# Performance work log

Measured on AMD Instinct MI355X. Metric: run time of the kernel, lower is better.

Reference implementation:

```python
import jax, jax.numpy as jnp
import numpy as np

B, N, D = 256, 196, 1024   # batch, regions, vis_embed_dim
HID, ATT, SIN, WID, ISD = 1024, 256, 1024, 1024, 256
S = 10                      # sentence steps


def _lin(key, out_dim, in_dim):
    kw, kb = jax.random.split(key)
    w = jax.random.normal(kw, (out_dim, in_dim), jnp.float32) * 0.02
    b = jax.random.normal(kb, (out_dim,), jnp.float32) * 0.02
    return w, b


def setup_inputs() -> dict:
    key = jax.random.key(0)
    ks = jax.random.split(key, 16)
    inp = {}
    inp['vis_enc'] = jax.random.normal(ks[0], (B, N, D), jnp.float32)
    inp['sentences'] = jax.random.randint(ks[1], (B, S, 50), 0, 10000, jnp.int64)
    inp['enc_att_w'], inp['enc_att_b'] = _lin(ks[2], ATT, D)
    inp['dec_att_w'], inp['dec_att_b'] = _lin(ks[3], ATT, HID)
    inp['full_att_w'], inp['full_att_b'] = _lin(ks[4], 1, ATT)
    inp['ctx_w'], inp['ctx_b'] = _lin(ks[5], SIN, D)
    inp['W_ih'], inp['b_ih'] = _lin(ks[6], 4 * HID, SIN)
    inp['W_hh'], inp['b_hh'] = _lin(ks[7], 4 * HID, HID)
    inp['topic_hid_w'], inp['topic_hid_b'] = _lin(ks[8], WID, HID)
    inp['topic_ctx_w'], inp['topic_ctx_b'] = _lin(ks[9], WID, SIN)
    inp['stop_prev_w'], inp['stop_prev_b'] = _lin(ks[10], ISD, HID)
    inp['stop_cur_w'], inp['stop_cur_b'] = _lin(ks[11], ISD, HID)
    inp['final_stop_w'], inp['final_stop_b'] = _lin(ks[12], 2, ISD)
    return inp


def reference(vis_enc, sentences,
              enc_att_w, enc_att_b, dec_att_w, dec_att_b, full_att_w, full_att_b,
              ctx_w, ctx_b, W_ih, b_ih, W_hh, b_hh,
              topic_hid_w, topic_hid_b, topic_ctx_w, topic_ctx_b,
              stop_prev_w, stop_prev_b, stop_cur_w, stop_cur_b,
              final_stop_w, final_stop_b):
    batch, hid = vis_enc.shape[0], W_hh.shape[1]
    sent_num = sentences.shape[1]
    # encoder projection is h-independent -> hoist out of the recurrence
    vis_enc_att = jnp.einsum('bnd,ad->bna', vis_enc, enc_att_w) + enc_att_b  # [B,N,ATT]

    def step(carry, _):
        h, c = carry
        # CoAtt additive attention
        dec = h @ dec_att_w.T + dec_att_b                       # [B,ATT]
        join = jnp.tanh(vis_enc_att + dec[:, None, :])          # [B,N,ATT]
        logits = jnp.einsum('bna,a->bn', join, full_att_w[0]) + full_att_b[0]
        scores = jax.nn.softmax(logits, axis=1)                 # [B,N]
        att_out = jnp.einsum('bn,bnd->bd', scores, vis_enc)     # [B,D]
        ctx = att_out @ ctx_w.T + ctx_b                         # [B,SIN]
        h_prev = h
        # LSTMCell
        gates = ctx @ W_ih.T + b_ih + h @ W_hh.T + b_hh         # [B,4H]
        i, f, g, o = jnp.split(gates, 4, axis=1)
        c_new = jax.nn.sigmoid(f) * c + jax.nn.sigmoid(i) * jnp.tanh(g)
        h_new = jax.nn.sigmoid(o) * jnp.tanh(c_new)
        # topic + stop heads
        topic = jnp.tanh(h_new @ topic_hid_w.T + topic_hid_b
                         + ctx @ topic_ctx_w.T + topic_ctx_b)   # [B,WID]
        p = jnp.tanh(h_prev @ stop_prev_w.T + stop_prev_b
                     + h_new @ stop_cur_w.T + stop_cur_b)
        p = p @ final_stop_w.T + final_stop_b                   # [B,2]
        return (h_new, c_new), (topic, p)

    h0 = jnp.zeros((batch, hid), vis_enc.dtype)
    c0 = jnp.zeros((batch, hid), vis_enc.dtype)
    _, (topics, ps) = jax.lax.scan(step, (h0, c0), None, length=sent_num)
    topics = jnp.transpose(topics, (1, 0, 2))  # [B,S,WID]
    ps = jnp.transpose(ps, (1, 0, 2))          # [B,S,2]
    return topics, ps
```

## Files before the change

### kernel.cpp

```cpp
#include <hip/hip_runtime.h>
#include <hip/hip_bf16.h>
#include <math.h>

static constexpr int BB = 256;
static constexpr int NR = 196;
static constexpr int DV = 1024;
static constexpr int HH = 1024;
static constexpr int AT = 256;
static constexpr int SI = 1024;
static constexpr int WI = 1024;
static constexpr int IS = 256;
static constexpr int ST = 10;

__device__ __forceinline__ float sigmoidf_(float x) { return 1.0f / (1.0f + expf(-x)); }

__device__ __forceinline__ ushort f2bf(float x) {
    uint u = __float_as_uint(x);
    return (ushort)((u + 0x7FFFu + ((u >> 16) & 1u)) >> 16);
}
__device__ __forceinline__ float bf2f(ushort b) { return __uint_as_float(((uint)b) << 16); }

using bf16x8 = __attribute__((ext_vector_type(8))) short;
using f32x4  = __attribute__((ext_vector_type(4))) float;
#define MFMA_B16(a, b, c) __builtin_amdgcn_mfma_f32_16x16x32_bf16((a), (b), (c), 0, 0, 0)

__device__ __forceinline__ void split8(const float4& u, const float4& v, uint4& hq, uint4& lq) {
    ushort h0 = f2bf(u.x), h1 = f2bf(u.y), h2 = f2bf(u.z), h3 = f2bf(u.w);
    ushort h4 = f2bf(v.x), h5 = f2bf(v.y), h6 = f2bf(v.z), h7 = f2bf(v.w);
    hq.x = h0 | ((uint)h1 << 16); hq.y = h2 | ((uint)h3 << 16);
    hq.z = h4 | ((uint)h5 << 16); hq.w = h6 | ((uint)h7 << 16);
    ushort l0 = f2bf(u.x - bf2f(h0)), l1 = f2bf(u.y - bf2f(h1));
    ushort l2 = f2bf(u.z - bf2f(h2)), l3 = f2bf(u.w - bf2f(h3));
    ushort l4 = f2bf(v.x - bf2f(h4)), l5 = f2bf(v.y - bf2f(h5));
    ushort l6 = f2bf(v.z - bf2f(h6)), l7 = f2bf(v.w - bf2f(h7));
    lq.x = l0 | ((uint)l1 << 16); lq.y = l2 | ((uint)l3 << 16);
    lq.z = l4 | ((uint)l5 << 16); lq.w = l6 | ((uint)l7 << 16);
}

struct CvtTab { const float* s[5]; ushort* h[5]; ushort* l[5]; };

__global__ __launch_bounds__(256) void convert_split(CvtTab tab) {
    const int cum[6] = {0, 256, 4352, 5376, 5632, 5888};
    const int bid = blockIdx.x;
    int seg = 0;
#pragma unroll
    for (int i = 1; i < 5; ++i) if (bid >= cum[i]) seg = i;
    const float* s = tab.s[seg];
    ushort* h = tab.h[seg];
    ushort* l = tab.l[seg];
    const int r = bid - cum[seg];
    int rd = r;
    if (seg == 1) rd = (r & 1023) * 4 + (r >> 10);
    const int src = r * 1024 + threadIdx.x * 4;
    const size_t dst = (size_t)rd * 1024 + threadIdx.x * 4;
    float4 v = *(const float4*)(s + src);
    ushort h0 = f2bf(v.x), h1 = f2bf(v.y), h2 = f2bf(v.z), h3 = f2bf(v.w);
    uint2 hq, lq;
    hq.x = h0 | ((uint)h1 << 16); hq.y = h2 | ((uint)h3 << 16);
    ushort l0 = f2bf(v.x - bf2f(h0)), l1 = f2bf(v.y - bf2f(h1));
    ushort l2 = f2bf(v.z - bf2f(h2)), l3 = f2bf(v.w - bf2f(h3));
    lq.x = l0 | ((uint)l1 << 16); lq.y = l2 | ((uint)l3 << 16);
    *(uint2*)(h + dst) = hq;
    *(uint2*)(l + dst) = lq;
}

__global__ __launch_bounds__(256) void convert_vis(
    const float* __restrict__ src, ushort* __restrict__ dst)
{
    const size_t i = ((size_t)blockIdx.x * 256 + threadIdx.x) * 8;
    const float4 v0 = *(const float4*)(src + i);
    const float4 v1 = *(const float4*)(src + i + 4);
    uint4 o;
    o.x = f2bf(v0.x) | ((uint)f2bf(v0.y) << 16);
    o.y = f2bf(v0.z) | ((uint)f2bf(v0.w) << 16);
    o.z = f2bf(v1.x) | ((uint)f2bf(v1.y) << 16);
    o.w = f2bf(v1.z) | ((uint)f2bf(v1.w) << 16);
    *(uint4*)(dst + i) = o;
}

__global__ __launch_bounds__(256) void transpose_split(
    const float* __restrict__ src, ushort* __restrict__ dh, ushort* __restrict__ dl)
{
    __shared__ float T[32][33];
    const int tx = threadIdx.x & 31, ty = threadIdx.x >> 5;
    const int k0 = blockIdx.x * 32, n0 = blockIdx.y * 32;
#pragma unroll
    for (int j = 0; j < 4; ++j)
        T[ty + 8 * j][tx] = src[(size_t)(k0 + ty + 8 * j) * 1024 + n0 + tx];
    __syncthreads();
#pragma unroll
    for (int j = 0; j < 4; ++j) {
        const float v = T[tx][ty + 8 * j];
        const ushort h = f2bf(v);
        const size_t o = (size_t)(n0 + ty + 8 * j) * 1024 + k0 + tx;
        dh[o] = h;
        dl[o] = f2bf(v - bf2f(h));
    }
}

__global__ __launch_bounds__(256) void foldbias(
    const float* __restrict__ W, const float* __restrict__ v,
    const float* __restrict__ b, float* __restrict__ out)
{
    const int n = blockIdx.x * 4 + (threadIdx.x >> 6);
    const int lane = threadIdx.x & 63;
    const float* wr = W + (size_t)n * 1024;
    float p = 0.f;
#pragma unroll
    for (int i = 0; i < 4; ++i) {
        const float4 wv = *(const float4*)&wr[i * 256 + lane * 4];
        const float4 vv = *(const float4*)&v[i * 256 + lane * 4];
        p = fmaf(wv.x, vv.x, p); p = fmaf(wv.y, vv.y, p);
        p = fmaf(wv.z, vv.z, p); p = fmaf(wv.w, vv.w, p);
    }
    for (int off = 32; off; off >>= 1) p += __shfl_down(p, off);
    if (lane == 0) out[n] = p + b[n];
}

template <int ILV>
__global__ __launch_bounds__(256) void mgemm_ws(
    const float* __restrict__ A, const ushort* __restrict__ Wh, const ushort* __restrict__ Wl,
    ushort* __restrict__ Ch, ushort* __restrict__ Cl, int N, int K)
{
    __shared__ __align__(16) ushort SM[4 * 64 * 40];
    ushort* Ah = SM; ushort* Al = SM + 2560; ushort* Bh = SM + 5120; ushort* Bl = SM + 7680;

    const int t = threadIdx.x;
    const int m0 = blockIdx.y * 64, n0 = blockIdx.x * 64;
    const int w = t >> 6, lane = t & 63;
    const int l15 = lane & 15, q = lane >> 4;
    const int sr = t >> 2, sq = (t & 3) * 8;
    const int nch = K >> 5;

    f32x4 acc[4] = {};
    float4 pa0, pa1; uint4 pbh, pbl;
    auto pref = [&](int c) {
        const int k0 = c << 5;
        const float* ap = &A[(size_t)(m0 + sr) * K + k0 + sq];
        pa0 = *(const float4*)ap;
        pa1 = *(const float4*)(ap + 4);
        pbh = *(const uint4*)&Wh[(size_t)(n0 + sr) * K + k0 + sq];
        pbl = *(const uint4*)&Wl[(size_t)(n0 + sr) * K + k0 + sq];
    };
    pref(0);

    for (int c = 0; c < nch; ++c) {
        __syncthreads();
        uint4 hq, lq; split8(pa0, pa1, hq, lq);
        *(uint4*)&Ah[sr * 40 + sq] = hq;
        *(uint4*)&Al[sr * 40 + sq] = lq;
        *(uint4*)&Bh[sr * 40 + sq] = pbh;
        *(uint4*)&Bl[sr * 40 + sq] = pbl;
        __syncthreads();
        if (c + 1 < nch) pref(c + 1);
        const bf16x8 bh = *(const bf16x8*)&Bh[(w * 16 + l15) * 40 + q * 8];
        const bf16x8 bl = *(const bf16x8*)&Bl[(w * 16 + l15) * 40 + q * 8];
#pragma unroll
        for (int mi = 0; mi < 4; ++mi) {
            const bf16x8 ah = *(const bf16x8*)&Ah[(mi * 16 + l15) * 40 + q * 8];
            const bf16x8 al = *(const bf16x8*)&Al[(mi * 16 + l15) * 40 + q * 8];
            acc[mi] = MFMA_B16(ah, bh, acc[mi]);
            acc[mi] = MFMA_B16(ah, bl, acc[mi]);
            acc[mi] = MFMA_B16(al, bh, acc[mi]);
        }
    }

    const int col = n0 + w * 16 + l15;
#pragma unroll
    for (int mi = 0; mi < 4; ++mi) {
#pragma unroll
        for (int j = 0; j < 4; ++j) {
            const int row = m0 + mi * 16 + q * 4 + j;
            const int ro = ILV ? ((row & 1023) * 4 + (row >> 10)) : row;
            const float v = acc[mi][j];
            const ushort h = f2bf(v);
            Ch[(size_t)ro * N + col] = h;
            Cl[(size_t)ro * N + col] = f2bf(v - bf2f(h));
        }
    }
}

template <int EPI, int DUAL, int OMAP>
__global__ __launch_bounds__(256) void mgemm(
    const float* __restrict__ A1, const ushort* __restrict__ W1h, const ushort* __restrict__ W1l,
    const float* __restrict__ b1,
    const float* __restrict__ A2, const ushort* __restrict__ W2h, const ushort* __restrict__ W2l,
    const float* __restrict__ b2,
    float* __restrict__ C, int M, int N, int K, int ldc)
{
    __shared__ __align__(16) ushort SM[4 * 64 * 40];
    ushort* Ah = SM; ushort* Al = SM + 2560; ushort* Bh = SM + 5120; ushort* Bl = SM + 7680;

    const int t = threadIdx.x;
    const int m0 = blockIdx.y * 64, n0 = blockIdx.x * 64;
    const int w = t >> 6, lane = t & 63;
    const int l15 = lane & 15, q = lane >> 4;
    const int sr = t >> 2, sq = (t & 3) * 8;
    const int KC = K >> 5, nch = (DUAL ? 2 : 1) * KC;

    f32x4 acc[4] = {};
    float4 pa0, pa1; uint4 pbh, pbl;

    auto pref = [&](int c) {
        const int pass = DUAL ? (c >= KC ? 1 : 0) : 0;
        const int k0 = (c - pass * KC) << 5;
        const float* A = pass ? A2 : A1;
        const ushort* Wh = pass ? W2h : W1h;
        const ushort* Wl = pass ? W2l : W1l;
        const float* ap = &A[(size_t)(m0 + sr) * K + k0 + sq];
        pa0 = *(const float4*)ap;
        pa1 = *(const float4*)(ap + 4);
        pbh = *(const uint4*)&Wh[(size_t)(n0 + sr) * K + k0 + sq];
        pbl = *(const uint4*)&Wl[(size_t)(n0 + sr) * K + k0 + sq];
    };
    pref(0);

    for (int c = 0; c < nch; ++c) {
        __syncthreads();
        uint4 hq, lq; split8(pa0, pa1, hq, lq);
        *(uint4*)&Ah[sr * 40 + sq] = hq;
        *(uint4*)&Al[sr * 40 + sq] = lq;
        *(uint4*)&Bh[sr * 40 + sq] = pbh;
        *(uint4*)&Bl[sr * 40 + sq] = pbl;
        __syncthreads();
        if (c + 1 < nch) pref(c + 1);
        const bf16x8 bh = *(const bf16x8*)&Bh[(w * 16 + l15) * 40 + q * 8];
        const bf16x8 bl = *(const bf16x8*)&Bl[(w * 16 + l15) * 40 + q * 8];
#pragma unroll
        for (int mi = 0; mi < 4; ++mi) {
            const bf16x8 ah = *(const bf16x8*)&Ah[(mi * 16 + l15) * 40 + q * 8];
            const bf16x8 al = *(const bf16x8*)&Al[(mi * 16 + l15) * 40 + q * 8];
            acc[mi] = MFMA_B16(ah, bh, acc[mi]);
            acc[mi] = MFMA_B16(ah, bl, acc[mi]);
            acc[mi] = MFMA_B16(al, bh, acc[mi]);
        }
    }

    const int col = n0 + w * 16 + l15;
    float bias = b1[col];
    if (DUAL) bias += b2[col];
#pragma unroll
    for (int mi = 0; mi < 4; ++mi) {
#pragma unroll
        for (int j = 0; j < 4; ++j) {
            const int row = m0 + mi * 16 + q * 4 + j;
            float v = acc[mi][j] + bias;
            if (EPI == 1) v = tanhf(v);
            if (OMAP)
                C[((size_t)(row & 255) * ST + (row >> 8)) * ldc + col] = v;
            else
                C[(size_t)row * ldc + col] = v;
        }
    }
}

__global__ __launch_bounds__(512) void mgemm8_lstm(
    const ushort* __restrict__ A1h, const ushort* __restrict__ A1l,
    const ushort* __restrict__ W1h, const ushort* __restrict__ W1l,
    const float* __restrict__ b1,
    const ushort* __restrict__ A2h, const ushort* __restrict__ A2l,
    const ushort* __restrict__ W2h, const ushort* __restrict__ W2l,
    const float* __restrict__ b2,
    int K, float* __restrict__ cvec, float* __restrict__ hnew,
    ushort* __restrict__ hnh, ushort* __restrict__ hnl)
{
    __shared__ __align__(16) ushort SM[32256];

    const int t = threadIdx.x;
    const int m0 = blockIdx.y * 64, n0 = blockIdx.x * 32;
    const int w = t >> 6, lane = t & 63;
    const int g = w >> 2, wg = w & 3;
    const int l15 = lane & 15, q = lane >> 4;
    const int tl = t & 255;
    const int sr = tl >> 2, sq4 = (tl & 3) * 16;
    const int br = tl >> 3, bq = (tl & 7) * 8;
    const int mh = wg >> 1;
    const int colL = (wg & 1) * 16 + l15;

    ushort* Ah = SM + g * 13824;
    ushort* Al = Ah + 4608;
    ushort* Bh = Al + 4608;
    ushort* Bl = Bh + 2304;

    const int nchg = K >> 6;
    const ushort* Ahg = g ? A2h : A1h;
    const ushort* Alg = g ? A2l : A1l;
    const ushort* Wh  = g ? W2h : W1h;
    const ushort* Wl  = g ? W2l : W1l;

    f32x4 acc[2] = {};
    uint4 pah0, pah1, pal0, pal1, pbh, pbl;
    auto pref = [&](int c) {
        const int k0 = c << 6;
        const size_t ab = (size_t)(m0 + sr) * K + k0 + sq4;
        pah0 = *(const uint4*)&Ahg[ab];
        pah1 = *(const uint4*)&Ahg[ab + 8];
        pal0 = *(const uint4*)&Alg[ab];
        pal1 = *(const uint4*)&Alg[ab + 8];
        pbh = *(const uint4*)&Wh[(size_t)(n0 + br) * K + k0 + bq];
        pbl = *(const uint4*)&Wl[(size_t)(n0 + br) * K + k0 + bq];
    };
    pref(0);

    for (int c = 0; c < nchg; ++c) {
        __syncthreads();
        *(uint4*)&Ah[sr * 72 + sq4]     = pah0;
        *(uint4*)&Ah[sr * 72 + sq4 + 8] = pah1;
        *(uint4*)&Al[sr * 72 + sq4]     = pal0;
        *(uint4*)&Al[sr * 72 + sq4 + 8] = pal1;
        *(uint4*)&Bh[br * 72 + bq] = pbh;
        *(uint4*)&Bl[br * 72 + bq] = pbl;
        __syncthreads();
        if (c + 1 < nchg) pref(c + 1);
#pragma unroll
        for (int ks = 0; ks < 2; ++ks) {
            const bf16x8 bh = *(const bf16x8*)&Bh[colL * 72 + ks * 32 + q * 8];
            const bf16x8 bl = *(const bf16x8*)&Bl[colL * 72 + ks * 32 + q * 8];
#pragma unroll
            for (int i = 0; i < 2; ++i) {
                const int mi = mh * 2 + i;
                const bf16x8 ah = *(const bf16x8*)&Ah[(mi * 16 + l15) * 72 + ks * 32 + q * 8];
                const bf16x8 al = *(const bf16x8*)&Al[(mi * 16 + l15) * 72 + ks * 32 + q * 8];
                acc[i] = MFMA_B16(ah, bh, acc[i]);
                acc[i] = MFMA_B16(ah, bl, acc[i]);
                acc[i] = MFMA_B16(al, bh, acc[i]);
            }
        }
    }

    float* comb = (float*)(SM + 27648);
    __syncthreads();
    if (g == 1) {
#pragma unroll
        for (int i = 0; i < 2; ++i)
#pragma unroll
            for (int j = 0; j < 4; ++j) comb[tl * 9 + i * 4 + j] = acc[i][j];
    }
    __syncthreads();
    if (g == 0) {
#pragma unroll
        for (int i = 0; i < 2; ++i)
#pragma unroll
            for (int j = 0; j < 4; ++j) acc[i][j] += comb[tl * 9 + i * 4 + j];
    }

    float* G = (float*)(SM + 13824);
    if (g == 0) {
        const int colG = n0 + colL;
        const int gate = colG & 3, unit = colG >> 2;
        const float bias = b1[gate * 1024 + unit] + b2[gate * 1024 + unit];
#pragma unroll
        for (int i = 0; i < 2; ++i) {
            const int mi = mh * 2 + i;
#pragma unroll
            for (int j = 0; j < 4; ++j)
                G[(mi * 16 + q * 4 + j) * 40 + colL] = acc[i][j] + bias;
        }
    }
    __syncthreads();
    {
        const int row = t >> 3, ul = t & 7;
        const float4 g4 = *(const float4*)&G[row * 40 + ul * 4];
        const size_t ci = (size_t)(m0 + row) * HH + (n0 >> 2) + ul;
        const float cn = sigmoidf_(g4.y) * cvec[ci] + sigmoidf_(g4.x) * tanhf(g4.z);
        cvec[ci] = cn;
        const float hv = sigmoidf_(g4.w) * tanhf(cn);
        hnew[ci] = hv;
        const ushort hhi = f2bf(hv);
        hnh[ci] = hhi;
        hnl[ci] = f2bf(hv - bf2f(hhi));
    }
}

__global__ __launch_bounds__(256) void mgemm_preb(
    const ushort* __restrict__ vh, const ushort* __restrict__ Wh, const ushort* __restrict__ Wl,
    const float* __restrict__ bias, ushort* __restrict__ C)
{
    __shared__ __align__(16) ushort Avh[64 * 40];
    __shared__ __align__(16) ushort Bh[256 * 40];
    __shared__ __align__(16) ushort Bl[256 * 40];

    const int t = threadIdx.x;
    const int m0 = blockIdx.x * 64;
    const int w = t >> 6, lane = t & 63;
    const int l15 = lane & 15, q = lane >> 4;
    const int ar = t >> 2, ac = (t & 3) * 8;
    const int K = DV;

    f32x4 acc[4][4] = {};

    for (int c = 0; c < 32; ++c) {
        const int k0 = c << 5;
        __syncthreads();
        *(uint4*)&Avh[ar * 40 + ac] = *(const uint4*)&vh[(size_t)(m0 + ar) * K + k0 + ac];
#pragma unroll
        for (int j = 0; j < 4; ++j) {
            const int r = j * 64 + (t >> 2);
            *(uint4*)&Bh[r * 40 + ac] = *(const uint4*)&Wh[(size_t)r * K + k0 + ac];
            *(uint4*)&Bl[r * 40 + ac] = *(const uint4*)&Wl[(size_t)r * K + k0 + ac];
        }
        __syncthreads();

        bf16x8 ah[4];
#pragma unroll
        for (int mi = 0; mi < 4; ++mi)
            ah[mi] = *(const bf16x8*)&Avh[(mi * 16 + l15) * 40 + q * 8];
#pragma unroll
        for (int ni = 0; ni < 4; ++ni) {
            const bf16x8 bh = *(const bf16x8*)&Bh[(w * 64 + ni * 16 + l15) * 40 + q * 8];
            const bf16x8 bl = *(const bf16x8*)&Bl[(w * 64 + ni * 16 + l15) * 40 + q * 8];
#pragma unroll
            for (int mi = 0; mi < 4; ++mi) {
                acc[mi][ni] = MFMA_B16(ah[mi], bh, acc[mi][ni]);
                acc[mi][ni] = MFMA_B16(ah[mi], bl, acc[mi][ni]);
            }
        }
    }

#pragma unroll
    for (int ni = 0; ni < 4; ++ni) {
        const int col = w * 64 + ni * 16 + l15;
        const float bb = bias[col];
#pragma unroll
        for (int mi = 0; mi < 4; ++mi)
#pragma unroll
            for (int j = 0; j < 4; ++j) {
                const int row = m0 + mi * 16 + q * 4 + j;
                C[(size_t)row * AT + col] = f2bf(acc[mi][ni][j] + bb);
            }
    }
}

__global__ __launch_bounds__(256) void mgemm_pre(
    const float* __restrict__ A, const ushort* __restrict__ Wh, const ushort* __restrict__ Wl,
    const float* __restrict__ bias, ushort* __restrict__ C)
{
    __shared__ __align__(16) ushort Ah[64 * 40], Al[64 * 40];
    __shared__ __align__(16) ushort Bh[256 * 40], Bl[256 * 40];

    const int t = threadIdx.x;
    const int m0 = blockIdx.x * 64;
    const int w = t >> 6, lane = t & 63;
    const int l15 = lane & 15, q = lane >> 4;
    const int sr = t >> 2, sq = (t & 3) * 8;
    const int K = DV;

    f32x4 acc[4][4] = {};
    float4 pa0, pa1;
    auto prefA = [&](int k0) {
        const float* ap = &A[(size_t)(m0 + sr) * K + k0 + sq];
        pa0 = *(const float4*)ap;
        pa1 = *(const float4*)(ap + 4);
    };
    prefA(0);

    for (int c = 0; c < 32; ++c) {
        const int k0 = c << 5;
        __syncthreads();
        uint4 hq, lq; split8(pa0, pa1, hq, lq);
        *(uint4*)&Ah[sr * 40 + sq] = hq;
        *(uint4*)&Al[sr * 40 + sq] = lq;
#pragma unroll
        for (int i = 0; i < 4; ++i) {
            const int r = sr + 64 * i;
            *(uint4*)&Bh[r * 40 + sq] = *(const uint4*)&Wh[(size_t)r * K + k0 + sq];
            *(uint4*)&Bl[r * 40 + sq] = *(const uint4*)&Wl[(size_t)r * K + k0 + sq];
        }
        __syncthreads();
        if (c + 1 < 32) prefA((c + 1) << 5);

        bf16x8 ah[4], al[4];
#pragma unroll
        for (int mi = 0; mi < 4; ++mi) {
            ah[mi] = *(const bf16x8*)&Ah[(mi * 16 + l15) * 40 + q * 8];
            al[mi] = *(const bf16x8*)&Al[(mi * 16 + l15) * 40 + q * 8];
        }
#pragma unroll
        for (int ni = 0; ni < 4; ++ni) {
            const bf16x8 bh = *(const bf16x8*)&Bh[(w * 64 + ni * 16 + l15) * 40 + q * 8];
            const bf16x8 bl = *(const bf16x8*)&Bl[(w * 64 + ni * 16 + l15) * 40 + q * 8];
#pragma unroll
            for (int mi = 0; mi < 4; ++mi) {
                acc[mi][ni] = MFMA_B16(ah[mi], bh, acc[mi][ni]);
                acc[mi][ni] = MFMA_B16(ah[mi], bl, acc[mi][ni]);
                acc[mi][ni] = MFMA_B16(al[mi], bh, acc[mi][ni]);
            }
        }
    }

#pragma unroll
    for (int ni = 0; ni < 4; ++ni) {
        const int col = w * 64 + ni * 16 + l15;
        const float bb = bias[col];
#pragma unroll
        for (int mi = 0; mi < 4; ++mi)
#pragma unroll
            for (int j = 0; j < 4; ++j) {
                const int row = m0 + mi * 16 + q * 4 + j;
                C[(size_t)row * AT + col] = f2bf(acc[mi][ni][j] + bb);
            }
    }
}

template <int VBF>
__global__ __launch_bounds__(1024) void att_step(
    const ushort* __restrict__ vis_att, const float* __restrict__ h,
    const float* __restrict__ dec_w, const float* __restrict__ dec_b,
    const float* __restrict__ fw, const float* __restrict__ fbp,
    const void* __restrict__ visp, float* __restrict__ att_out,
    ushort* __restrict__ att_h, ushort* __restrict__ att_l)
{
    const int b = blockIdx.x;
    const int t = threadIdx.x;
    const int lane = t & 63;
    const int w = t >> 6;

    __shared__ float hs[HH];
    __shared__ float decs[AT];
    __shared__ float fwv[AT];
    __shared__ float logit[NR + 4];
    __shared__ float sc[NR + 4];
    __shared__ float red[8];
    __shared__ float part[8][DV];

    hs[t] = h[(size_t)b * HH + t];
    if (t < AT) fwv[t] = fw[t];
    __syncthreads();
    const float fb = fbp[0];

#pragma unroll
    for (int j = 0; j < 16; ++j) {
        const int a = w * 16 + j;
        const float* wr = dec_w + (size_t)a * HH;
        float p = 0.f;
#pragma unroll
        for (int i = 0; i < 4; ++i) {
            const float4 wv = *(const float4*)&wr[i * 256 + lane * 4];
            const float4 hv = *(const float4*)&hs[i * 256 + lane * 4];
            p = fmaf(wv.x, hv.x, p); p = fmaf(wv.y, hv.y, p);
            p = fmaf(wv.z, hv.z, p); p = fmaf(wv.w, hv.w, p);
        }
        for (int off = 32; off; off >>= 1) p += __shfl_down(p, off);
        if (lane == 0) decs[a] = p + dec_b[a];
    }
    __syncthreads();

    for (int n = w; n < NR; n += 16) {
        const ushort4 v4 = *(const ushort4*)&vis_att[((size_t)b * NR + n) * AT + lane * 4];
        const int a = lane * 4;
        float s = tanhf(bf2f(v4.x) + decs[a]) * fwv[a];
        s = fmaf(tanhf(bf2f(v4.y) + decs[a + 1]), fwv[a + 1], s);
        s = fmaf(tanhf(bf2f(v4.z) + decs[a + 2]), fwv[a + 2], s);
        s = fmaf(tanhf(bf2f(v4.w) + decs[a + 3]), fwv[a + 3], s);
        for (int off = 32; off; off >>= 1) s += __shfl_down(s, off);
        if (lane == 0) logit[n] = s + fb;
    }
    __syncthreads();

    float m = -1e30f, e = 0.f;
    if (t < NR) m = logit[t];
    if (t < 256) {
        for (int off = 32; off; off >>= 1) m = fmaxf(m, __shfl_down(m, off));
        if (lane == 0) red[w] = m;
    }
    __syncthreads();
    m = fmaxf(fmaxf(red[0], red[1]), fmaxf(red[2], red[3]));
    if (t < NR) e = expf(logit[t] - m);
    if (t < 256) {
        float ss = e;
        for (int off = 32; off; off >>= 1) ss += __shfl_down(ss, off);
        if (lane == 0) red[4 + w] = ss;
    }
    __syncthreads();
    const float S = red[4] + red[5] + red[6] + red[7];
    if (t < NR) sc[t] = e / S;
    __syncthreads();

    const int slice = t >> 7;
    const int c8 = (t & 127) * 8;
    const int nbeg = (slice <= 4) ? 25 * slice : 100 + 24 * (slice - 4);
    const int nend = (slice < 4) ? nbeg + 25 : nbeg + 24;
    float a0 = 0.f, a1 = 0.f, a2 = 0.f, a3 = 0.f;
    float a4 = 0.f, a5 = 0.f, a6 = 0.f, a7 = 0.f;
    if (VBF) {
        const ushort* vb = (const ushort*)visp + (size_t)b * NR * DV + c8;
        for (int n = nbeg; n < nend; ++n) {
            const float s = sc[n];
            const uint4 v = *(const uint4*)&vb[(size_t)n * DV];
            a0 = fmaf(s, bf2f((ushort)(v.x & 0xFFFF)), a0);
            a1 = fmaf(s, bf2f((ushort)(v.x >> 16)), a1);
            a2 = fmaf(s, bf2f((ushort)(v.y & 0xFFFF)), a2);
            a3 = fmaf(s, bf2f((ushort)(v.y >> 16)), a3);
            a4 = fmaf(s, bf2f((ushort)(v.z & 0xFFFF)), a4);
            a5 = fmaf(s, bf2f((ushort)(v.z >> 16)), a5);
            a6 = fmaf(s, bf2f((ushort)(v.w & 0xFFFF)), a6);
            a7 = fmaf(s, bf2f((ushort)(v.w >> 16)), a7);
        }
    } else {
        const float* vb = (const float*)visp + (size_t)b * NR * DV + c8;
        for (int n = nbeg; n < nend; ++n) {
            const float s = sc[n];
            const float4 v0 = *(const float4*)&vb[(size_t)n * DV];
            const float4 v1 = *(const float4*)&vb[(size_t)n * DV + 4];
            a0 = fmaf(s, v0.x, a0); a1 = fmaf(s, v0.y, a1);
            a2 = fmaf(s, v0.z, a2); a3 = fmaf(s, v0.w, a3);
            a4 = fmaf(s, v1.x, a4); a5 = fmaf(s, v1.y, a5);
            a6 = fmaf(s, v1.z, a6); a7 = fmaf(s, v1.w, a7);
        }
    }
    float4 av0; av0.x = a0; av0.y = a1; av0.z = a2; av0.w = a3;
    float4 av1; av1.x = a4; av1.y = a5; av1.z = a6; av1.w = a7;
    *(float4*)&part[slice][c8]     = av0;
    *(float4*)&part[slice][c8 + 4] = av1;
    __syncthreads();
    const float v = ((part[0][t] + part[1][t]) + (part[2][t] + part[3][t]))
                  + ((part[4][t] + part[5][t]) + (part[6][t] + part[7][t]));
    att_out[(size_t)b * DV + t] = v;
    const ushort vh16 = f2bf(v);
    att_h[(size_t)b * DV + t] = vh16;
    att_l[(size_t)b * DV + t] = f2bf(v - bf2f(vh16));
}

__global__ __launch_bounds__(256) void stop_final_all(
    const float* __restrict__ pt, const float* __restrict__ fw,
    const float* __restrict__ fb, float* __restrict__ outp)
{
    const int row = blockIdx.x;
    const int s = row >> 8, b = row & 255;
    const int t = threadIdx.x;
    const int lane = t & 63;
    const int w = t >> 6;

    __shared__ float red[16];
    const float v = pt[(size_t)row * IS + t];
    float p0 = v * fw[t];
    float p1 = v * fw[IS + t];
    for (int off = 32; off; off >>= 1) {
        p0 += __shfl_down(p0, off);
        p1 += __shfl_down(p1, off);
    }
    if (lane == 0) { red[w] = p0; red[8 + w] = p1; }
    __syncthreads();
    if (t == 0) {
        outp[((size_t)b * ST + s) * 2 + 0] = red[0] + red[1] + red[2] + red[3] + fb[0];
        outp[((size_t)b * ST + s) * 2 + 1] = red[8] + red[9] + red[10] + red[11] + fb[1];
    }
}

extern "C" void kernel_launch(void* const* d_in, const int* in_sizes, int n_in,
                              void* d_out, int out_size, void* d_ws, size_t ws_size,
                              hipStream_t stream)
{
    const float* vis        = (const float*)d_in[0];
    const float* enc_att_w  = (const float*)d_in[2];
    const float* enc_att_b  = (const float*)d_in[3];
    const float* dec_att_w  = (const float*)d_in[4];
    const float* dec_att_b  = (const float*)d_in[5];
    const float* full_att_w = (const float*)d_in[6];
    const float* full_att_b = (const float*)d_in[7];
    const float* ctx_w      = (const float*)d_in[8];
    const float* ctx_b      = (const float*)d_in[9];
    const float* W_ih       = (const float*)d_in[10];
    const float* b_ih       = (const float*)d_in[11];
    const float* W_hh       = (const float*)d_in[12];
    const float* b_hh       = (const float*)d_in[13];
    const float* topic_hid_w = (const float*)d_in[14];
    const float* topic_hid_b = (const float*)d_in[15];
    const float* topic_ctx_w = (const float*)d_in[16];
    const float* topic_ctx_b = (const float*)d_in[17];
    const float* stop_prev_w = (const float*)d_in[18];
    const float* stop_prev_b = (const float*)d_in[19];
    const float* stop_cur_w  = (const float*)d_in[20];
    const float* stop_cur_b  = (const float*)d_in[21];
    const float* final_stop_w = (const float*)d_in[22];
    const float* final_stop_b = (const float*)d_in[23];

    float* out_topics = (float*)d_out;
    float* out_ps     = (float*)d_out + (size_t)BB * ST * WI;

    char* ws = (char*)d_ws;
    size_t off = 0;
    auto alloc = [&](size_t bytes) -> void* {
        void* p = (void*)(ws + off);
        off += (bytes + 255) & ~(size_t)255;
        return p;
    };
    ushort* vis_att = (ushort*)alloc((size_t)BB * NR * AT * 2);
    const size_t WTOT = (size_t)5888 * 1024;
    ushort* wh = (ushort*)alloc(WTOT * 2);
    ushort* wl = (ushort*)alloc(WTOT * 2);
    float* h_all   = (float*)alloc((size_t)(ST + 1) * BB * HH * 4);
    ushort* hh_h   = (ushort*)alloc((size_t)(ST + 1) * BB * HH * 2);
    ushort* hh_l   = (ushort*)alloc((size_t)(ST + 1) * BB * HH * 2);
    float* att_all = (float*)alloc((size_t)ST * BB * DV * 4);
    ushort* att_h  = (ushort*)alloc((size_t)BB * DV * 2);
    ushort* att_l  = (ushort*)alloc((size_t)BB * DV * 2);
    float* cbuf    = (float*)alloc((size_t)BB * HH * 4);
    float* pt_all  = (float*)alloc((size_t)ST * BB * IS * 4);
    ushort* ctT_h  = (ushort*)alloc((size_t)SI * DV * 2);
    ushort* ctT_l  = (ushort*)alloc((size_t)SI * DV * 2);
    ushort* cmb_h  = (ushort*)alloc((size_t)4 * HH * SI * 2);
    ushort* cmb_l  = (ushort*)alloc((size_t)4 * HH * SI * 2);
    ushort* tcc_h  = (ushort*)alloc((size_t)WI * SI * 2);
    ushort* tcc_l  = (ushort*)alloc((size_t)WI * SI * 2);
    float* bf_ih   = (float*)alloc((size_t)4 * HH * 4);
    float* bf_tc   = (float*)alloc((size_t)WI * 4);
    if (off > ws_size) return;
    ushort* vis_bf = nullptr;
    {
        const size_t need = (size_t)BB * NR * DV * 2;
        if (off + need <= ws_size) vis_bf = (ushort*)alloc(need);
    }

    const size_t O_ENC = 0;
    const size_t O_HH  = 262144;
    const size_t O_TH  = 4456448;
    const size_t O_SP  = 5505024;
    const size_t O_SC  = 5767168;

    CvtTab tab;
    const float* srcs[5] = {enc_att_w, W_hh, topic_hid_w, stop_prev_w, stop_cur_w};
    const size_t offs[5] = {O_ENC, O_HH, O_TH, O_SP, O_SC};
    for (int i = 0; i < 5; ++i) {
        tab.s[i] = srcs[i];
        tab.h[i] = wh + offs[i];
        tab.l[i] = wl + offs[i];
    }

    hipMemsetAsync(h_all, 0, (size_t)BB * HH * 4, stream);
    hipMemsetAsync(hh_h, 0, (size_t)BB * HH * 2, stream);
    hipMemsetAsync(hh_l, 0, (size_t)BB * HH * 2, stream);
    hipMemsetAsync(cbuf, 0, (size_t)BB * HH * 4, stream);

    convert_split<<<5888, 256, 0, stream>>>(tab);

    transpose_split<<<dim3(SI / 32, DV / 32), 256, 0, stream>>>(ctx_w, ctT_h, ctT_l);
    mgemm_ws<1><<<dim3(SI / 64, 4 * HH / 64), 256, 0, stream>>>(
        W_ih, ctT_h, ctT_l, cmb_h, cmb_l, SI, DV);
    mgemm_ws<0><<<dim3(SI / 64, WI / 64), 256, 0, stream>>>(
        topic_ctx_w, ctT_h, ctT_l, tcc_h, tcc_l, SI, DV);
    foldbias<<<(4 * HH) / 4, 256, 0, stream>>>(W_ih, ctx_b, b_ih, bf_ih);
    foldbias<<<WI / 4, 256, 0, stream>>>(topic_ctx_w, ctx_b, topic_ctx_b, bf_tc);

    if (vis_bf) {
        convert_vis<<<(BB * NR * DV) / (256 * 8), 256, 0, stream>>>(vis, vis_bf);
        mgemm_preb<<<(BB * NR) / 64, 256, 0, stream>>>(
            vis_bf, wh + O_ENC, wl + O_ENC, enc_att_b, vis_att);
    } else {
        mgemm_pre<<<(BB * NR) / 64, 256, 0, stream>>>(
            vis, wh + O_ENC, wl + O_ENC, enc_att_b, vis_att);
    }

    for (int s = 0; s < ST; ++s) {
        float* hc = h_all + (size_t)s * BB * HH;
        float* hn = h_all + (size_t)(s + 1) * BB * HH;
        ushort* hch = hh_h + (size_t)s * BB * HH;
        ushort* hcl = hh_l + (size_t)s * BB * HH;
        ushort* hnh = hh_h + (size_t)(s + 1) * BB * HH;
        ushort* hnl = hh_l + (size_t)(s + 1) * BB * HH;
        float* atts = att_all + (size_t)s * BB * DV;
        if (vis_bf)
            att_step<1><<<BB, 1024, 0, stream>>>(vis_att, hc, dec_att_w, dec_att_b,
                                                 full_att_w, full_att_b, vis_bf, atts,
                                                 att_h, att_l);
        else
            att_step<0><<<BB, 1024, 0, stream>>>(vis_att, hc, dec_att_w, dec_att_b,
                                                 full_att_w, full_att_b, vis, atts,
                                                 att_h, att_l);
        mgemm8_lstm<<<dim3(4 * HH / 32, BB / 64), 512, 0, stream>>>(
            att_h, att_l, cmb_h, cmb_l, bf_ih,
            hch, hcl, wh + O_HH, wl + O_HH, b_hh,
            SI, cbuf, hn, hnh, hnl);
    }

    mgemm<1, 1, 1><<<dim3(WI / 64, (ST * BB) / 64), 256, 0, stream>>>(
        h_all + (size_t)BB * HH, wh + O_TH, wl + O_TH, topic_hid_b,
        att_all, tcc_h, tcc_l, bf_tc,
        out_topics, ST * BB, WI, HH, WI);
    mgemm<1, 1, 0><<<dim3(IS / 64, (ST * BB) / 64), 256, 0, stream>>>(
        h_all, wh + O_SP, wl + O_SP, stop_prev_b,
        h_all + (size_t)BB * HH, wh + O_SC, wl + O_SC, stop_cur_b,
        pt_all, ST * BB, IS, HH, IS);
    stop_final_all<<<ST * BB, 256, 0, stream>>>(pt_all, final_stop_w, final_stop_b, out_ps);
}
```

Baseline: 1.099 ms.

## Enlarge encoder-projection GEMM tile to 128 rows and prefetch next K chunk

The bf16 encoder-attention projection kernel now uses 512 threads and a 128-row M tile, so each block shares the loaded weight tile (hi and lo parts) across twice as many rows. It also loads the next K chunk into registers before the current chunk's MFMAs, so global loads overlap with compute. This cuts redundant weight traffic from global memory, at the cost of more registers and half as many blocks. It only affects the one-time precompute ahead of the recurrence.

```diff
diff --git a/kernel.cpp b/kernel.cpp
--- a/kernel.cpp
+++ b/kernel.cpp
@@ -372,43 +372,54 @@
     }
 }
 
-__global__ __launch_bounds__(256) void mgemm_preb(
+__global__ __launch_bounds__(512) void mgemm_preb(
     const ushort* __restrict__ vh, const ushort* __restrict__ Wh, const ushort* __restrict__ Wl,
     const float* __restrict__ bias, ushort* __restrict__ C)
 {
-    __shared__ __align__(16) ushort Avh[64 * 40];
+    __shared__ __align__(16) ushort Avh[128 * 40];
     __shared__ __align__(16) ushort Bh[256 * 40];
     __shared__ __align__(16) ushort Bl[256 * 40];
 
     const int t = threadIdx.x;
-    const int m0 = blockIdx.x * 64;
+    const int m0 = blockIdx.x * 128;
     const int w = t >> 6, lane = t & 63;
+    const int rg = w >> 2, cg = w & 3;
     const int l15 = lane & 15, q = lane >> 4;
     const int ar = t >> 2, ac = (t & 3) * 8;
+    const int brr = t >> 1, bc = (t & 1) * 16;
     const int K = DV;
 
     f32x4 acc[4][4] = {};
+    uint4 pa, pbh0, pbh1, pbl0, pbl1;
+    auto pref = [&](int c) {
+        const int k0 = c << 5;
+        pa   = *(const uint4*)&vh[(size_t)(m0 + ar) * K + k0 + ac];
+        const size_t bb = (size_t)brr * K + k0 + bc;
+        pbh0 = *(const uint4*)&Wh[bb];
+        pbh1 = *(const uint4*)&Wh[bb + 8];
+        pbl0 = *(const uint4*)&Wl[bb];
+        pbl1 = *(const uint4*)&Wl[bb + 8];
+    };
+    pref(0);
 
     for (int c = 0; c < 32; ++c) {
-        const int k0 = c << 5;
-        __syncthreads();
-        *(uint4*)&Avh[ar * 40 + ac] = *(const uint4*)&vh[(size_t)(m0 + ar) * K + k0 + ac];
-#pragma unroll
-        for (int j = 0; j < 4; ++j) {
-            const int r = j * 64 + (t >> 2);
-            *(uint4*)&Bh[r * 40 + ac] = *(const uint4*)&Wh[(size_t)r * K + k0 + ac];
-            *(uint4*)&Bl[r * 40 + ac] = *(const uint4*)&Wl[(size_t)r * K + k0 + ac];
-        }
-        __syncthreads();
+        __syncthreads();
+        *(uint4*)&Avh[ar * 40 + ac] = pa;
+        *(uint4*)&Bh[brr * 40 + bc]     = pbh0;
+        *(uint4*)&Bh[brr * 40 + bc + 8] = pbh1;
+        *(uint4*)&Bl[brr * 40 + bc]     = pbl0;
+        *(uint4*)&Bl[brr * 40 + bc + 8] = pbl1;
+        __syncthreads();
+        if (c + 1 < 32) pref(c + 1);
 
         bf16x8 ah[4];
 #pragma unroll
         for (int mi = 0; mi < 4; ++mi)
-            ah[mi] = *(const bf16x8*)&Avh[(mi * 16 + l15) * 40 + q * 8];
+            ah[mi] = *(const bf16x8*)&Avh[(rg * 64 + mi * 16 + l15) * 40 + q * 8];
 #pragma unroll
         for (int ni = 0; ni < 4; ++ni) {
-            const bf16x8 bh = *(const bf16x8*)&Bh[(w * 64 + ni * 16 + l15) * 40 + q * 8];
-            const bf16x8 bl = *(const bf16x8*)&Bl[(w * 64 + ni * 16 + l15) * 40 + q * 8];
+            const bf16x8 bh = *(const bf16x8*)&Bh[(cg * 64 + ni * 16 + l15) * 40 + q * 8];
+            const bf16x8 bl = *(const bf16x8*)&Bl[(cg * 64 + ni * 16 + l15) * 40 + q * 8];
 #pragma unroll
             for (int mi = 0; mi < 4; ++mi) {
                 acc[mi][ni] = MFMA_B16(ah[mi], bh, acc[mi][ni]);
@@ -419,13 +430,13 @@
 
 #pragma unroll
     for (int ni = 0; ni < 4; ++ni) {
-        const int col = w * 64 + ni * 16 + l15;
+        const int col = cg * 64 + ni * 16 + l15;
         const float bb = bias[col];
 #pragma unroll
         for (int mi = 0; mi < 4; ++mi)
 #pragma unroll
             for (int j = 0; j < 4; ++j) {
-                const int row = m0 + mi * 16 + q * 4 + j;
+                const int row = m0 + rg * 64 + mi * 16 + q * 4 + j;
                 C[(size_t)row * AT + col] = f2bf(acc[mi][ni][j] + bb);
             }
     }
@@ -744,7 +755,7 @@
 
     if (vis_bf) {
         convert_vis<<<(BB * NR * DV) / (256 * 8), 256, 0, stream>>>(vis, vis_bf);
-        mgemm_preb<<<(BB * NR) / 64, 256, 0, stream>>>(
+        mgemm_preb<<<(BB * NR) / 128, 512, 0, stream>>>(
             vis_bf, wh + O_ENC, wl + O_ENC, enc_att_b, vis_att);
     } else {
         mgemm_pre<<<(BB * NR) / 64, 256, 0, stream>>>(
```

Result: faster. 1.073 ms (-2.3%).
